# Performance work log

Measured on AMD Instinct MI355X. Metric: run time of the kernel, lower is better.

Reference implementation:

```python
import jax, jax.numpy as jnp
import numpy as np

B = 524288
D_IN = 128
H = 16          # hard-coded by amax slicing in MLSTMCell
D_OUT = 4


def _quant(x, amax):
    # torch quant_tensor: clamp(round(x * 127/amax), -127, 127) -> int8 (kept as
    # integer-valued float32 here; exact since |v| <= 127)
    if amax.ndim > 1:
        amax = jnp.squeeze(amax, 1)
    return jnp.clip(jnp.round(x * (127.0 / amax)), -127.0, 127.0)


def _dequant(x, amax, double=False):
    max_range = 127.0 ** 2 if double else 127.0
    scale = max_range / amax
    if scale.ndim > 1:
        scale = jnp.squeeze(scale, 1)
    return x / scale


def setup_inputs() -> dict:
    key = jax.random.key(0)
    ks = jax.random.split(key, 13)
    # weights are stored pre-quantized int8 (integer-valued); torch casts them
    # to int32 before matmul, so integer-valued float32 is bit-exact in fp32
    intw = lambda k, shp: jax.random.randint(k, shp, -127, 128).astype(jnp.float32)
    x = jax.random.normal(ks[0], (B, D_IN), dtype=jnp.float32)
    h = jax.random.normal(ks[1], (B, H), dtype=jnp.float32) * 0.1
    c = jax.random.normal(ks[2], (B, H), dtype=jnp.float32) * 0.1
    w1 = intw(ks[3], (H, D_IN))          # net.0.weight
    w_ih = intw(ks[4], (4 * H, H))       # lstm.weight_ih
    w_hh = intw(ks[5], (4 * H, H))       # lstm.weight_hh
    w_out = intw(ks[6], (D_OUT, H))      # output_layer.weight
    u = lambda k, shp, lo, hi: jax.random.uniform(k, shp, minval=lo, maxval=hi, dtype=jnp.float32)
    amax_in0 = u(ks[7], (), 1.0, 4.0)            # net.0._input_quantizer._amax (per-tensor)
    amax_w0 = u(ks[8], (H, 1), 32.0, 127.0)      # net.0._weight_quantizer._amax (per-channel)
    amax_lstm_in = u(ks[9], (), 1.0, 4.0)        # lstm._input_quantizer._amax
    amax_w_lstm = u(ks[10], (4 * H, 1), 32.0, 127.0)  # lstm._weight_quantizer._amax
    amax_out_in = u(ks[11], (), 1.0, 4.0)        # output_layer._input_quantizer._amax
    amax_w_out = u(ks[12], (D_OUT, 1), 32.0, 127.0)   # output_layer._weight_quantizer._amax
    return dict(x=x, h=h, c=c, w1=w1, w_ih=w_ih, w_hh=w_hh, w_out=w_out,
                amax_in0=amax_in0, amax_w0=amax_w0, amax_lstm_in=amax_lstm_in,
                amax_w_lstm=amax_w_lstm, amax_out_in=amax_out_in, amax_w_out=amax_w_out)


def reference(x, h, c, w1, w_ih, w_hh, w_out, amax_in0, amax_w0,
              amax_lstm_in, amax_w_lstm, amax_out_in, amax_w_out):
    # --- fc_1: quantize input, int matmul, relu, requantize for lstm ---
    xq = _quant(x, amax_in0)                     # [B, D_IN] int8-valued
    a = xq @ w1.T                                # [B, H] int32-valued (exact in fp32)
    a = jnp.maximum(a, 0.0)                      # relu
    a = _quant(_dequant(a, amax_in0 * amax_w0, double=True), amax_lstm_in)  # [B, H]
    # --- quantize hidden state (hc arrives as float) ---
    hq = _quant(h, amax_lstm_in)
    cq = _quant(c, amax_lstm_in)
    # --- MLSTMCell ---
    amax = amax_lstm_in * amax_w_lstm            # [4H, 1]
    gates = a @ w_ih.T + hq @ w_hh.T             # [B, 4H] int32-valued
    gates = _dequant(gates, amax, double=True)
    i, f, g, o = jnp.split(gates, 4, axis=1)
    gates = jnp.concatenate([jax.nn.sigmoid(i), jax.nn.sigmoid(f),
                             jnp.tanh(g), jax.nn.sigmoid(o)], axis=1)
    gq = _quant(gates, amax)                     # [B, 4H] int8-valued
    i, f, g, o = jnp.split(gq, 4, axis=1)
    cy = (_dequant(f * cq, amax[16:32] * 3.4764, double=True)
          + _dequant(i * g, amax[:16] * amax[32:48], double=True))
    od = _dequant(o, amax[48:], double=False)
    hy = od * jnp.tanh(cy)
    # --- output layer ---
    xo = _quant(hy, amax_out_in) @ w_out.T       # [B, D_OUT]
    xo = _dequant(xo, amax_out_in * amax_w_out, double=True)
    return xo, hy, cy
```

## Files before the change

### kernel.cpp

```cpp
#include <hip/hip_runtime.h>
#include <math.h>
#include <limits.h>


#define OFF_QS    0
#define OFF_SFC1  4
#define OFF_SG    20
#define OFF_QG    84
#define OFF_SCF   148
#define OFF_SCIG  164
#define OFF_SOD   180
#define OFF_SXO   196
#define OFF_VBG   200
#define OFF_TI    216
#define OFF_TF    280
#define OFF_TO    344
#define OFF_TG    408
#define OFF_IGT   536
#define OFF_ODT   1064
#define OFF_W1P   1192
#define OFF_WIHP  1704
#define OFF_WHHP  1960
#define OFF_WOUTP 2216

__device__ __forceinline__ float qclip(float v) {
    return fminf(fmaxf(v, -127.0f), 127.0f);
}

__device__ __forceinline__ int sdot4(int a, int b, int c) {
#if __has_builtin(__builtin_amdgcn_sdot4)
    return __builtin_amdgcn_sdot4(a, b, c, false);
#else
    c += ((a << 24) >> 24) * ((b << 24) >> 24);
    c += ((a << 16) >> 24) * ((b << 16) >> 24);
    c += ((a << 8)  >> 24) * ((b << 8)  >> 24);
    c += (a >> 24) * (b >> 24);
    return c;
#endif
}

__device__ __forceinline__ int pack4i(int a, int b, int c, int d) {
    return (a & 255) | ((b & 255) << 8) | ((c & 255) << 16) | (d << 24);
}

__device__ __forceinline__ int pack4f(const float* p) {
    return pack4i((int)p[0], (int)p[1], (int)p[2], (int)p[3]);
}

__device__ __forceinline__ int quantpack(float4 v, float qs) {
    return pack4i((int)qclip(rintf(v.x * qs)), (int)qclip(rintf(v.y * qs)),
                  (int)qclip(rintf(v.z * qs)), (int)qclip(rintf(v.w * qs)));
}

#define WAIT_LGKM0() { asm volatile("s_waitcnt lgkmcnt(0)" ::: "memory"); __builtin_amdgcn_sched_barrier(0); }

__device__ __forceinline__ int qeval_sig(int gi, float s, float q) {
    float v = (float)gi / s;
    float a = 1.0f / (1.0f + expf(-v));
    return (int)qclip(rintf(a * q));
}
__device__ __forceinline__ int qeval_tanh(int gi, float s, float q) {
    float v = (float)gi / s;
    float a = tanhf(v);
    return (int)qclip(rintf(a * q));
}

#define GLIM 1048576

__device__ int search_thr_sig(float s, float q, int target) {
    if (qeval_sig(GLIM, s, q) < target) return INT_MAX;
    int lo = -GLIM, hi = GLIM;
    while (hi - lo > 1) {
        int mid = lo + ((hi - lo) >> 1);
        if (qeval_sig(mid, s, q) >= target) hi = mid; else lo = mid;
    }
    return hi;
}
__device__ int search_thr_tanh(float s, float q, int target) {
    if (qeval_tanh(GLIM, s, q) < target) return INT_MAX;
    int lo = -GLIM, hi = GLIM;
    while (hi - lo > 1) {
        int mid = lo + ((hi - lo) >> 1);
        if (qeval_tanh(mid, s, q) >= target) hi = mid; else lo = mid;
    }
    return hi;
}

__global__ void __launch_bounds__(1024) setup_all(
    const float* __restrict__ w1, const float* __restrict__ w_ih,
    const float* __restrict__ w_hh, const float* __restrict__ w_out,
    const float* __restrict__ a_in0, const float* __restrict__ a_w0,
    const float* __restrict__ a_lstm, const float* __restrict__ a_wl,
    const float* __restrict__ a_out, const float* __restrict__ a_wo,
    float* __restrict__ wsf)
{
    const int t = threadIdx.x;
    int* wsi = (int*)wsf;
    const float amax_in0 = a_in0[0], amax_lstm = a_lstm[0], amax_out = a_out[0];

    if (t == 0) {
        wsf[OFF_QS + 0] = 127.0f / amax_in0;
        wsf[OFF_QS + 1] = 127.0f / amax_lstm;
        wsf[OFF_QS + 2] = 127.0f / amax_out;
    }
    if (t < 16) wsf[OFF_SFC1 + t] = 16129.0f / (amax_in0 * a_w0[t]);
    if (t < 64) {
        float am = amax_lstm * a_wl[t];
        wsf[OFF_SG + t] = 16129.0f / am;
        wsf[OFF_QG + t] = 127.0f / am;
    }
    if (t < 16) {
        float amf = amax_lstm * a_wl[16 + t];
        wsf[OFF_SCF + t] = 16129.0f / (amf * 3.4764f);
        float amo = amax_lstm * a_wl[48 + t];
        wsf[OFF_SOD + t] = 127.0f / amo;
        float ami = amax_lstm * a_wl[t];
        float amg = amax_lstm * a_wl[32 + t];
        wsf[OFF_SCIG + t] = 16129.0f / (ami * amg);
        float s = 16129.0f / amg, q = 127.0f / amg;
        wsi[OFF_VBG + t] = qeval_tanh(-GLIM, s, q);
    }
    if (t < 4) wsf[OFF_SXO + t] = 16129.0f / (amax_out * a_wo[t]);

    if (t < 512) wsi[OFF_W1P + t] = pack4f(w1 + 4 * t);
    if (t < 256) { wsi[OFF_WIHP + t] = pack4f(w_ih + 4 * t);
                   wsi[OFF_WHHP + t] = pack4f(w_hh + 4 * t); }
    if (t < 16)  wsi[OFF_WOUTP + t] = pack4f(w_out + 4 * t);

    if (t < 64) {
        int m = t >> 2, k = t & 3;
        float am = amax_lstm * a_wl[m];
        wsi[OFF_TI + t] = search_thr_sig(16129.0f / am, 127.0f / am, k + 1);
    } else if (t < 128) {
        int u = t - 64, m = u >> 2, k = u & 3;
        float am = amax_lstm * a_wl[16 + m];
        wsi[OFF_TF + u] = search_thr_sig(16129.0f / am, 127.0f / am, k + 1);
    } else if (t < 192) {
        int u = t - 128, m = u >> 2, k = u & 3;
        float am = amax_lstm * a_wl[48 + m];
        wsi[OFF_TO + u] = search_thr_sig(16129.0f / am, 127.0f / am, k + 1);
    } else if (t < 320) {
        int u = t - 192, m = u >> 3, k = u & 7;
        float am = amax_lstm * a_wl[32 + m];
        float s = 16129.0f / am, q = 127.0f / am;
        int vb = qeval_tanh(-GLIM, s, q);
        wsi[OFF_TG + u] = search_thr_tanh(s, q, vb + 1 + k);
    } else if (t < 848) {
        int u = t - 320, m = u / 33, p = u % 33;
        float ami = amax_lstm * a_wl[m];
        float amg = amax_lstm * a_wl[32 + m];
        float scig = 16129.0f / (ami * amg);
        wsf[OFF_IGT + u] = (float)(p - 16) / scig;
    } else if (t < 928) {
        int u = t - 848, m = u / 5, oq = u % 5;
        float amo = amax_lstm * a_wl[48 + m];
        float sod = 127.0f / amo;
        wsf[OFF_ODT + m * 8 + oq] = (float)oq / sod;
    }
}

__global__ void __launch_bounds__(256, 4) mlpq_kernel(
    const float* __restrict__ x, const float* __restrict__ h, const float* __restrict__ c,
    const float* __restrict__ wsf,
    float* __restrict__ out_xo, float* __restrict__ out_hy, float* __restrict__ out_cy,
    int nrows)
{
    __shared__ float s_tab[656];
    __shared__ __align__(16) int s_xq[4][2048];

    for (int i = threadIdx.x; i < 656; i += 256) s_tab[i] = wsf[OFF_IGT + i];
    __syncthreads();
    const float* s_igt = s_tab;
    const float* s_odt = s_tab + 528;

    const int tid = threadIdx.x;
    const int wv  = tid >> 6;
    const int rl  = tid & 63;
    const int wrow0 = blockIdx.x * 256 + wv * 64;
    const int r = wrow0 + rl;

    const int qd = rl & 3;
    const int g  = rl >> 2;

    int* bufi = &s_xq[wv][0];

    const int* __restrict__ wsi = (const int*)wsf;
    const float qs_in   = wsf[OFF_QS + 0];
    const float qs_lstm = wsf[OFF_QS + 1];
    const float qs_out  = wsf[OFF_QS + 2];

    const float4* __restrict__ xb = reinterpret_cast<const float4*>(x);

    float4 xr0[8], xr1[8];
    {
        const size_t ro = (size_t)(wrow0 + 0 * 16 + g) * 32 + qd;
#pragma unroll
        for (int s = 0; s < 8; ++s) xr0[s] = xb[ro + s * 4];
    }
    {
        const size_t ro = (size_t)(wrow0 + 1 * 16 + g) * 32 + qd;
#pragma unroll
        for (int s = 0; s < 8; ++s) xr1[s] = xb[ro + s * 4];
    }

#define PROC_SUBITER(I, REG, RELOAD)                                         \
    {                                                                        \
        const int rp  = (I) * 16 + g;                                        \
        const int wb  = rp * 32;                                             \
        const int swz = (rp & 7) << 2;                                       \
        int pw[8];                                                           \
        _Pragma("unroll")                                                    \
        for (int s = 0; s < 8; ++s) pw[s] = quantpack(REG[s], qs_in);        \
        _Pragma("unroll")                                                    \
        for (int s = 0; s < 8; ++s)                                          \
            bufi[wb + ((s * 4 + qd) ^ swz)] = pw[s];                         \
        if (RELOAD) {                                                        \
            const size_t ro2 = (size_t)(wrow0 + ((I) + 2) * 16 + g) * 32 + qd;\
            _Pragma("unroll")                                                \
            for (int s = 0; s < 8; ++s) REG[s] = xb[ro2 + s * 4];            \
        }                                                                    \
    }

    PROC_SUBITER(0, xr0, 1)
    PROC_SUBITER(1, xr1, 1)
    PROC_SUBITER(2, xr0, 0)
    PROC_SUBITER(3, xr1, 0)
#undef PROC_SUBITER

    float4 hv4[4], cv4[4];
    {
        const float4* hb = reinterpret_cast<const float4*>(h) + (size_t)r * 4;
        const float4* cb = reinterpret_cast<const float4*>(c) + (size_t)r * 4;
#pragma unroll
        for (int jg = 0; jg < 4; ++jg) { hv4[jg] = hb[jg]; cv4[jg] = cb[jg]; }
    }

    WAIT_LGKM0();

    int xw[32];
    {
        const int4* b4 = reinterpret_cast<const int4*>(bufi);
#pragma unroll
        for (int t = 0; t < 8; ++t) {
            int4 vv = b4[rl * 8 + (t ^ (rl & 7))];
            xw[t * 4 + 0] = vv.x; xw[t * 4 + 1] = vv.y;
            xw[t * 4 + 2] = vv.z; xw[t * 4 + 3] = vv.w;
        }
    }

    int acc[16];
#pragma unroll
    for (int j = 0; j < 16; ++j) {
        int a = 0;
        const int* wrow = wsi + OFF_W1P + j * 32;
#pragma unroll
        for (int k = 0; k < 32; ++k) a = sdot4(xw[k], wrow[k], a);
        acc[j] = a;
    }

    int aql[4];
#pragma unroll
    for (int jg = 0; jg < 4; ++jg) {
        int qv[4];
#pragma unroll
        for (int u = 0; u < 4; ++u) {
            int j = jg * 4 + u;
            int ai = acc[j] > 0 ? acc[j] : 0;
            float dq = (float)ai / wsf[OFF_SFC1 + j];
            qv[u] = (int)qclip(rintf(dq * qs_lstm));
        }
        aql[jg] = pack4i(qv[0], qv[1], qv[2], qv[3]);
    }

    int hql[4];
#pragma unroll
    for (int jg = 0; jg < 4; ++jg) hql[jg] = quantpack(hv4[jg], qs_lstm);

    float4* __restrict__ hyrow = reinterpret_cast<float4*>(out_hy) + (size_t)r * 4;
    float4* __restrict__ cyrow = reinterpret_cast<float4*>(out_cy) + (size_t)r * 4;
    int xql[4];

#pragma unroll
    for (int mg = 0; mg < 4; ++mg) {
        float4 cv = cv4[mg];
        float cvals[4] = {cv.x, cv.y, cv.z, cv.w};
        float hy4[4], cy4[4];
        int xq4[4];
#pragma unroll
        for (int t = 0; t < 4; ++t) {
            const int m = mg * 4 + t;
            int gi = 0, gf = 0, gg = 0, go = 0;
#pragma unroll
            for (int p = 0; p < 4; ++p) {
                int ap = aql[p], hp = hql[p];
                gi = sdot4(ap, wsi[OFF_WIHP + (m)      * 4 + p], gi);
                gi = sdot4(hp, wsi[OFF_WHHP + (m)      * 4 + p], gi);
                gf = sdot4(ap, wsi[OFF_WIHP + (m + 16) * 4 + p], gf);
                gf = sdot4(hp, wsi[OFF_WHHP + (m + 16) * 4 + p], gf);
                gg = sdot4(ap, wsi[OFF_WIHP + (m + 32) * 4 + p], gg);
                gg = sdot4(hp, wsi[OFF_WHHP + (m + 32) * 4 + p], gg);
                go = sdot4(ap, wsi[OFF_WIHP + (m + 48) * 4 + p], go);
                go = sdot4(hp, wsi[OFF_WHHP + (m + 48) * 4 + p], go);
            }
            int iq = (gi >= wsi[OFF_TI + m * 4 + 0]) + (gi >= wsi[OFF_TI + m * 4 + 1])
                   + (gi >= wsi[OFF_TI + m * 4 + 2]) + (gi >= wsi[OFF_TI + m * 4 + 3]);
            int fq = (gf >= wsi[OFF_TF + m * 4 + 0]) + (gf >= wsi[OFF_TF + m * 4 + 1])
                   + (gf >= wsi[OFF_TF + m * 4 + 2]) + (gf >= wsi[OFF_TF + m * 4 + 3]);
            int oq = (go >= wsi[OFF_TO + m * 4 + 0]) + (go >= wsi[OFF_TO + m * 4 + 1])
                   + (go >= wsi[OFF_TO + m * 4 + 2]) + (go >= wsi[OFF_TO + m * 4 + 3]);
            int gq = wsi[OFF_VBG + m]
                   + (gg >= wsi[OFF_TG + m * 8 + 0]) + (gg >= wsi[OFF_TG + m * 8 + 1])
                   + (gg >= wsi[OFF_TG + m * 8 + 2]) + (gg >= wsi[OFF_TG + m * 8 + 3])
                   + (gg >= wsi[OFF_TG + m * 8 + 4]) + (gg >= wsi[OFF_TG + m * 8 + 5])
                   + (gg >= wsi[OFF_TG + m * 8 + 6]) + (gg >= wsi[OFF_TG + m * 8 + 7]);

            int cqv = (int)qclip(rintf(cvals[t] * qs_lstm));

            float cy = (float)(fq * cqv) / wsf[OFF_SCF + m]
                     + s_igt[m * 33 + (iq * gq + 16)];
            float od = s_odt[m * 8 + oq];
            float hy = od * tanhf(cy);

            hy4[t] = hy;
            cy4[t] = cy;
            xq4[t] = (int)qclip(rintf(hy * qs_out));
        }
        hyrow[mg] = make_float4(hy4[0], hy4[1], hy4[2], hy4[3]);
        cyrow[mg] = make_float4(cy4[0], cy4[1], cy4[2], cy4[3]);
        xql[mg] = pack4i(xq4[0], xq4[1], xq4[2], xq4[3]);
    }

    float4 xov;
    {
        int s0 = 0, s1 = 0, s2 = 0, s3 = 0;
#pragma unroll
        for (int p = 0; p < 4; ++p) {
            s0 = sdot4(xql[p], wsi[OFF_WOUTP + 0 * 4 + p], s0);
            s1 = sdot4(xql[p], wsi[OFF_WOUTP + 1 * 4 + p], s1);
            s2 = sdot4(xql[p], wsi[OFF_WOUTP + 2 * 4 + p], s2);
            s3 = sdot4(xql[p], wsi[OFF_WOUTP + 3 * 4 + p], s3);
        }
        xov.x = (float)s0 / wsf[OFF_SXO + 0];
        xov.y = (float)s1 / wsf[OFF_SXO + 1];
        xov.z = (float)s2 / wsf[OFF_SXO + 2];
        xov.w = (float)s3 / wsf[OFF_SXO + 3];
    }
    reinterpret_cast<float4*>(out_xo)[r] = xov;
}

extern "C" void kernel_launch(void* const* d_in, const int* in_sizes, int n_in,
                              void* d_out, int out_size, void* d_ws, size_t ws_size,
                              hipStream_t stream) {
    const float* x      = (const float*)d_in[0];
    const float* h      = (const float*)d_in[1];
    const float* c      = (const float*)d_in[2];
    const float* w1     = (const float*)d_in[3];
    const float* w_ih   = (const float*)d_in[4];
    const float* w_hh   = (const float*)d_in[5];
    const float* w_out  = (const float*)d_in[6];
    const float* a_in0  = (const float*)d_in[7];
    const float* a_w0   = (const float*)d_in[8];
    const float* a_lstm = (const float*)d_in[9];
    const float* a_wl   = (const float*)d_in[10];
    const float* a_out  = (const float*)d_in[11];
    const float* a_wo   = (const float*)d_in[12];

    const int B = in_sizes[0] / 128;
    float* out    = (float*)d_out;
    float* out_xo = out;
    float* out_hy = out + (size_t)B * 4;
    float* out_cy = out + (size_t)B * 20;
    float* wsf    = (float*)d_ws;

    hipLaunchKernelGGL(setup_all, dim3(1), dim3(1024), 0, stream,
                       w1, w_ih, w_hh, w_out, a_in0, a_w0, a_lstm, a_wl, a_out, a_wo, wsf);

    dim3 block(256);
    dim3 grid((B + 255) / 256);
    hipLaunchKernelGGL(mlpq_kernel, grid, block, 0, stream,
                       x, h, c, wsf, out_xo, out_hy, out_cy, B);
}
```

Before: 120.2 us.

## Process four rows per thread with register double-buffered direct x loads

Drops the LDS transpose of quantized x. Each thread now loads its own row's x directly in 8-float4 chunks, double-buffered in registers, and accumulates the first-layer dot products chunk by chunk. Each thread handles four rows in a loop, so the grid shrinks fourfold and the launch-bounds occupancy hint is removed. The trade-off is uncoalesced per-thread row loads (each lane reads a 512-byte stride), fewer waves in flight to hide latency, and a grid that assumes B is divisible by 1024.

```diff
diff --git a/kernel.cpp b/kernel.cpp
--- a/kernel.cpp
+++ b/kernel.cpp
@@ -51,8 +51,6 @@
     return pack4i((int)qclip(rintf(v.x * qs)), (int)qclip(rintf(v.y * qs)),
                   (int)qclip(rintf(v.z * qs)), (int)qclip(rintf(v.w * qs)));
 }
-
-#define WAIT_LGKM0() { asm volatile("s_waitcnt lgkmcnt(0)" ::: "memory"); __builtin_amdgcn_sched_barrier(0); }
 
 __device__ __forceinline__ int qeval_sig(int gi, float s, float q) {
     float v = (float)gi / s;
@@ -159,30 +157,22 @@
     }
 }
 
-__global__ void __launch_bounds__(256, 4) mlpq_kernel(
+#define ROWS_PER_THREAD 4
+
+__global__ void __launch_bounds__(256) mlpq_kernel(
     const float* __restrict__ x, const float* __restrict__ h, const float* __restrict__ c,
     const float* __restrict__ wsf,
     float* __restrict__ out_xo, float* __restrict__ out_hy, float* __restrict__ out_cy,
     int nrows)
 {
     __shared__ float s_tab[656];
-    __shared__ __align__(16) int s_xq[4][2048];
-
     for (int i = threadIdx.x; i < 656; i += 256) s_tab[i] = wsf[OFF_IGT + i];
     __syncthreads();
     const float* s_igt = s_tab;
     const float* s_odt = s_tab + 528;
 
     const int tid = threadIdx.x;
-    const int wv  = tid >> 6;
-    const int rl  = tid & 63;
-    const int wrow0 = blockIdx.x * 256 + wv * 64;
-    const int r = wrow0 + rl;
-
-    const int qd = rl & 3;
-    const int g  = rl >> 2;
-
-    int* bufi = &s_xq[wv][0];
+    const int rowbase = blockIdx.x * (256 * ROWS_PER_THREAD);
 
     const int* __restrict__ wsi = (const int*)wsf;
     const float qs_in   = wsf[OFF_QS + 0];
@@ -190,162 +180,147 @@
     const float qs_out  = wsf[OFF_QS + 2];
 
     const float4* __restrict__ xb = reinterpret_cast<const float4*>(x);
-
-    float4 xr0[8], xr1[8];
+    const float4* __restrict__ hb = reinterpret_cast<const float4*>(h);
+    const float4* __restrict__ cb = reinterpret_cast<const float4*>(c);
+
+    float4 xf[8], xg[8];
     {
-        const size_t ro = (size_t)(wrow0 + 0 * 16 + g) * 32 + qd;
-#pragma unroll
-        for (int s = 0; s < 8; ++s) xr0[s] = xb[ro + s * 4];
-    }
-    {
-        const size_t ro = (size_t)(wrow0 + 1 * 16 + g) * 32 + qd;
-#pragma unroll
-        for (int s = 0; s < 8; ++s) xr1[s] = xb[ro + s * 4];
-    }
-
-#define PROC_SUBITER(I, REG, RELOAD)                                         \
-    {                                                                        \
-        const int rp  = (I) * 16 + g;                                        \
-        const int wb  = rp * 32;                                             \
-        const int swz = (rp & 7) << 2;                                       \
-        int pw[8];                                                           \
-        _Pragma("unroll")                                                    \
-        for (int s = 0; s < 8; ++s) pw[s] = quantpack(REG[s], qs_in);        \
-        _Pragma("unroll")                                                    \
-        for (int s = 0; s < 8; ++s)                                          \
-            bufi[wb + ((s * 4 + qd) ^ swz)] = pw[s];                         \
-        if (RELOAD) {                                                        \
-            const size_t ro2 = (size_t)(wrow0 + ((I) + 2) * 16 + g) * 32 + qd;\
-            _Pragma("unroll")                                                \
-            for (int s = 0; s < 8; ++s) REG[s] = xb[ro2 + s * 4];            \
-        }                                                                    \
-    }
-
-    PROC_SUBITER(0, xr0, 1)
-    PROC_SUBITER(1, xr1, 1)
-    PROC_SUBITER(2, xr0, 0)
-    PROC_SUBITER(3, xr1, 0)
-#undef PROC_SUBITER
-
-    float4 hv4[4], cv4[4];
-    {
-        const float4* hb = reinterpret_cast<const float4*>(h) + (size_t)r * 4;
-        const float4* cb = reinterpret_cast<const float4*>(c) + (size_t)r * 4;
-#pragma unroll
-        for (int jg = 0; jg < 4; ++jg) { hv4[jg] = hb[jg]; cv4[jg] = cb[jg]; }
-    }
-
-    WAIT_LGKM0();
-
-    int xw[32];
-    {
-        const int4* b4 = reinterpret_cast<const int4*>(bufi);
-#pragma unroll
-        for (int t = 0; t < 8; ++t) {
-            int4 vv = b4[rl * 8 + (t ^ (rl & 7))];
-            xw[t * 4 + 0] = vv.x; xw[t * 4 + 1] = vv.y;
-            xw[t * 4 + 2] = vv.z; xw[t * 4 + 3] = vv.w;
+        const size_t xr0 = (size_t)(rowbase + tid) * 32;
+#pragma unroll
+        for (int s = 0; s < 8; ++s) xf[s] = xb[xr0 + s];
+    }
+
+#pragma unroll 1
+    for (int it = 0; it < ROWS_PER_THREAD; ++it) {
+        const int r = rowbase + it * 256 + tid;
+        const size_t xrow = (size_t)r * 32;
+
+        int acc[16];
+#pragma unroll
+        for (int j = 0; j < 16; ++j) acc[j] = 0;
+        float4 hv4[4], cv4[4];
+
+#pragma unroll
+        for (int ch = 0; ch < 4; ++ch) {
+            float4* cur = (ch & 1) ? xg : xf;
+            float4* nxt = (ch & 1) ? xf : xg;
+            if (ch < 3) {
+#pragma unroll
+                for (int s = 0; s < 8; ++s) nxt[s] = xb[xrow + (ch + 1) * 8 + s];
+            } else if (it < ROWS_PER_THREAD - 1) {
+                const size_t nx = (size_t)(r + 256) * 32;
+#pragma unroll
+                for (int s = 0; s < 8; ++s) nxt[s] = xb[nx + s];
+            }
+            if (ch == 2) {
+#pragma unroll
+                for (int jg = 0; jg < 4; ++jg) {
+                    hv4[jg] = hb[(size_t)r * 4 + jg];
+                    cv4[jg] = cb[(size_t)r * 4 + jg];
+                }
+            }
+            int pw[8];
+#pragma unroll
+            for (int s = 0; s < 8; ++s) pw[s] = quantpack(cur[s], qs_in);
+#pragma unroll
+            for (int j = 0; j < 16; ++j) {
+                int a = acc[j];
+                const int* wr = wsi + OFF_W1P + j * 32 + ch * 8;
+#pragma unroll
+                for (int s = 0; s < 8; ++s) a = sdot4(pw[s], wr[s], a);
+                acc[j] = a;
+            }
         }
-    }
-
-    int acc[16];
-#pragma unroll
-    for (int j = 0; j < 16; ++j) {
-        int a = 0;
-        const int* wrow = wsi + OFF_W1P + j * 32;
-#pragma unroll
-        for (int k = 0; k < 32; ++k) a = sdot4(xw[k], wrow[k], a);
-        acc[j] = a;
-    }
-
-    int aql[4];
-#pragma unroll
-    for (int jg = 0; jg < 4; ++jg) {
-        int qv[4];
-#pragma unroll
-        for (int u = 0; u < 4; ++u) {
-            int j = jg * 4 + u;
-            int ai = acc[j] > 0 ? acc[j] : 0;
-            float dq = (float)ai / wsf[OFF_SFC1 + j];
-            qv[u] = (int)qclip(rintf(dq * qs_lstm));
+
+        int aql[4];
+#pragma unroll
+        for (int jg = 0; jg < 4; ++jg) {
+            int qv[4];
+#pragma unroll
+            for (int u = 0; u < 4; ++u) {
+                int j = jg * 4 + u;
+                int ai = acc[j] > 0 ? acc[j] : 0;
+                float dq = (float)ai / wsf[OFF_SFC1 + j];
+                qv[u] = (int)qclip(rintf(dq * qs_lstm));
+            }
+            aql[jg] = pack4i(qv[0], qv[1], qv[2], qv[3]);
         }
-        aql[jg] = pack4i(qv[0], qv[1], qv[2], qv[3]);
-    }
-
-    int hql[4];
-#pragma unroll
-    for (int jg = 0; jg < 4; ++jg) hql[jg] = quantpack(hv4[jg], qs_lstm);
-
-    float4* __restrict__ hyrow = reinterpret_cast<float4*>(out_hy) + (size_t)r * 4;
-    float4* __restrict__ cyrow = reinterpret_cast<float4*>(out_cy) + (size_t)r * 4;
-    int xql[4];
-
-#pragma unroll
-    for (int mg = 0; mg < 4; ++mg) {
-        float4 cv = cv4[mg];
-        float cvals[4] = {cv.x, cv.y, cv.z, cv.w};
-        float hy4[4], cy4[4];
-        int xq4[4];
-#pragma unroll
-        for (int t = 0; t < 4; ++t) {
-            const int m = mg * 4 + t;
-            int gi = 0, gf = 0, gg = 0, go = 0;
+
+        int hql[4];
+#pragma unroll
+        for (int jg = 0; jg < 4; ++jg) hql[jg] = quantpack(hv4[jg], qs_lstm);
+
+        float4* __restrict__ hyrow = reinterpret_cast<float4*>(out_hy) + (size_t)r * 4;
+        float4* __restrict__ cyrow = reinterpret_cast<float4*>(out_cy) + (size_t)r * 4;
+        int xql[4];
+
+#pragma unroll
+        for (int mg = 0; mg < 4; ++mg) {
+            float4 cv = cv4[mg];
+            float cvals[4] = {cv.x, cv.y, cv.z, cv.w};
+            float hy4[4], cy4[4];
+            int xq4[4];
+#pragma unroll
+            for (int t = 0; t < 4; ++t) {
+                const int m = mg * 4 + t;
+                int gi = 0, gf = 0, gg = 0, go = 0;
+#pragma unroll
+                for (int p = 0; p < 4; ++p) {
+                    int ap = aql[p], hp = hql[p];
+                    gi = sdot4(ap, wsi[OFF_WIHP + (m)      * 4 + p], gi);
+                    gi = sdot4(hp, wsi[OFF_WHHP + (m)      * 4 + p], gi);
+                    gf = sdot4(ap, wsi[OFF_WIHP + (m + 16) * 4 + p], gf);
+                    gf = sdot4(hp, wsi[OFF_WHHP + (m + 16) * 4 + p], gf);
+                    gg = sdot4(ap, wsi[OFF_WIHP + (m + 32) * 4 + p], gg);
+                    gg = sdot4(hp, wsi[OFF_WHHP + (m + 32) * 4 + p], gg);
+                    go = sdot4(ap, wsi[OFF_WIHP + (m + 48) * 4 + p], go);
+                    go = sdot4(hp, wsi[OFF_WHHP + (m + 48) * 4 + p], go);
+                }
+                int iq = (gi >= wsi[OFF_TI + m * 4 + 0]) + (gi >= wsi[OFF_TI + m * 4 + 1])
+                       + (gi >= wsi[OFF_TI + m * 4 + 2]) + (gi >= wsi[OFF_TI + m * 4 + 3]);
+                int fq = (gf >= wsi[OFF_TF + m * 4 + 0]) + (gf >= wsi[OFF_TF + m * 4 + 1])
+                       + (gf >= wsi[OFF_TF + m * 4 + 2]) + (gf >= wsi[OFF_TF + m * 4 + 3]);
+                int oq = (go >= wsi[OFF_TO + m * 4 + 0]) + (go >= wsi[OFF_TO + m * 4 + 1])
+                       + (go >= wsi[OFF_TO + m * 4 + 2]) + (go >= wsi[OFF_TO + m * 4 + 3]);
+                int gq = wsi[OFF_VBG + m]
+                       + (gg >= wsi[OFF_TG + m * 8 + 0]) + (gg >= wsi[OFF_TG + m * 8 + 1])
+                       + (gg >= wsi[OFF_TG + m * 8 + 2]) + (gg >= wsi[OFF_TG + m * 8 + 3])
+                       + (gg >= wsi[OFF_TG + m * 8 + 4]) + (gg >= wsi[OFF_TG + m * 8 + 5])
+                       + (gg >= wsi[OFF_TG + m * 8 + 6]) + (gg >= wsi[OFF_TG + m * 8 + 7]);
+
+                int cqv = (int)qclip(rintf(cvals[t] * qs_lstm));
+
+                float cy = (float)(fq * cqv) / wsf[OFF_SCF + m]
+                         + s_igt[m * 33 + (iq * gq + 16)];
+                float od = s_odt[m * 8 + oq];
+                float hy = od * tanhf(cy);
+
+                hy4[t] = hy;
+                cy4[t] = cy;
+                xq4[t] = (int)qclip(rintf(hy * qs_out));
+            }
+            hyrow[mg] = make_float4(hy4[0], hy4[1], hy4[2], hy4[3]);
+            cyrow[mg] = make_float4(cy4[0], cy4[1], cy4[2], cy4[3]);
+            xql[mg] = pack4i(xq4[0], xq4[1], xq4[2], xq4[3]);
+        }
+
+        float4 xov;
+        {
+            int s0 = 0, s1 = 0, s2 = 0, s3 = 0;
 #pragma unroll
             for (int p = 0; p < 4; ++p) {
-                int ap = aql[p], hp = hql[p];
-                gi = sdot4(ap, wsi[OFF_WIHP + (m)      * 4 + p], gi);
-                gi = sdot4(hp, wsi[OFF_WHHP + (m)      * 4 + p], gi);
-                gf = sdot4(ap, wsi[OFF_WIHP + (m + 16) * 4 + p], gf);
-                gf = sdot4(hp, wsi[OFF_WHHP + (m + 16) * 4 + p], gf);
-                gg = sdot4(ap, wsi[OFF_WIHP + (m + 32) * 4 + p], gg);
-                gg = sdot4(hp, wsi[OFF_WHHP + (m + 32) * 4 + p], gg);
-                go = sdot4(ap, wsi[OFF_WIHP + (m + 48) * 4 + p], go);
-                go = sdot4(hp, wsi[OFF_WHHP + (m + 48) * 4 + p], go);
-            }
-            int iq = (gi >= wsi[OFF_TI + m * 4 + 0]) + (gi >= wsi[OFF_TI + m * 4 + 1])
-                   + (gi >= wsi[OFF_TI + m * 4 + 2]) + (gi >= wsi[OFF_TI + m * 4 + 3]);
-            int fq = (gf >= wsi[OFF_TF + m * 4 + 0]) + (gf >= wsi[OFF_TF + m * 4 + 1])
-                   + (gf >= wsi[OFF_TF + m * 4 + 2]) + (gf >= wsi[OFF_TF + m * 4 + 3]);
-            int oq = (go >= wsi[OFF_TO + m * 4 + 0]) + (go >= wsi[OFF_TO + m * 4 + 1])
-                   + (go >= wsi[OFF_TO + m * 4 + 2]) + (go >= wsi[OFF_TO + m * 4 + 3]);
-            int gq = wsi[OFF_VBG + m]
-                   + (gg >= wsi[OFF_TG + m * 8 + 0]) + (gg >= wsi[OFF_TG + m * 8 + 1])
-                   + (gg >= wsi[OFF_TG + m * 8 + 2]) + (gg >= wsi[OFF_TG + m * 8 + 3])
-                   + (gg >= wsi[OFF_TG + m * 8 + 4]) + (gg >= wsi[OFF_TG + m * 8 + 5])
-                   + (gg >= wsi[OFF_TG + m * 8 + 6]) + (gg >= wsi[OFF_TG + m * 8 + 7]);
-
-            int cqv = (int)qclip(rintf(cvals[t] * qs_lstm));
-
-            float cy = (float)(fq * cqv) / wsf[OFF_SCF + m]
-                     + s_igt[m * 33 + (iq * gq + 16)];
-            float od = s_odt[m * 8 + oq];
-            float hy = od * tanhf(cy);
-
-            hy4[t] = hy;
-            cy4[t] = cy;
-            xq4[t] = (int)qclip(rintf(hy * qs_out));
+                s0 = sdot4(xql[p], wsi[OFF_WOUTP + 0 * 4 + p], s0);
+                s1 = sdot4(xql[p], wsi[OFF_WOUTP + 1 * 4 + p], s1);
+                s2 = sdot4(xql[p], wsi[OFF_WOUTP + 2 * 4 + p], s2);
+                s3 = sdot4(xql[p], wsi[OFF_WOUTP + 3 * 4 + p], s3);
+            }
+            xov.x = (float)s0 / wsf[OFF_SXO + 0];
+            xov.y = (float)s1 / wsf[OFF_SXO + 1];
+            xov.z = (float)s2 / wsf[OFF_SXO + 2];
+            xov.w = (float)s3 / wsf[OFF_SXO + 3];
         }
-        hyrow[mg] = make_float4(hy4[0], hy4[1], hy4[2], hy4[3]);
-        cyrow[mg] = make_float4(cy4[0], cy4[1], cy4[2], cy4[3]);
-        xql[mg] = pack4i(xq4[0], xq4[1], xq4[2], xq4[3]);
-    }
-
-    float4 xov;
-    {
-        int s0 = 0, s1 = 0, s2 = 0, s3 = 0;
-#pragma unroll
-        for (int p = 0; p < 4; ++p) {
-            s0 = sdot4(xql[p], wsi[OFF_WOUTP + 0 * 4 + p], s0);
-            s1 = sdot4(xql[p], wsi[OFF_WOUTP + 1 * 4 + p], s1);
-            s2 = sdot4(xql[p], wsi[OFF_WOUTP + 2 * 4 + p], s2);
-            s3 = sdot4(xql[p], wsi[OFF_WOUTP + 3 * 4 + p], s3);
-        }
-        xov.x = (float)s0 / wsf[OFF_SXO + 0];
-        xov.y = (float)s1 / wsf[OFF_SXO + 1];
-        xov.z = (float)s2 / wsf[OFF_SXO + 2];
-        xov.w = (float)s3 / wsf[OFF_SXO + 3];
-    }
-    reinterpret_cast<float4*>(out_xo)[r] = xov;
+        reinterpret_cast<float4*>(out_xo)[r] = xov;
+    }
 }
 
 extern "C" void kernel_launch(void* const* d_in, const int* in_sizes, int n_in,
@@ -376,7 +351,7 @@
                        w1, w_ih, w_hh, w_out, a_in0, a_w0, a_lstm, a_wl, a_out, a_wo, wsf);
 
     dim3 block(256);
-    dim3 grid((B + 255) / 256);
+    dim3 grid(B / (256 * ROWS_PER_THREAD));
     hipLaunchKernelGGL(mlpq_kernel, grid, block, 0, stream,
                        x, h, c, wsf, out_xo, out_hy, out_cy, B);
 }
```

Result: slower. 180.1 us (+49.9%).
